# Kernel tuning notes

Measured on AMD Instinct MI355X. Metric: run time of the kernel, lower is better.

## Reference

```python
import jax, jax.numpy as jnp
import numpy as np

B, Nq, C, H = 1, 300, 256, 8
h, w = 32, 32
HW = h * w
HID = 512  # rpe_hidden_dim
HD = C // H


def setup_inputs() -> dict:
    key = jax.random.key(0)
    ks = jax.random.split(key, 16)
    s = 0.02
    inp = {
        "raw_query": jax.random.normal(ks[0], (B, Nq, C), jnp.float32),
        "query_pos": jax.random.normal(ks[1], (B, Nq, C), jnp.float32),
        "reference_points": jax.random.uniform(ks[2], (B, Nq, 2), jnp.float32),
        "raw_src": jax.random.normal(ks[3], (B, HW, C), jnp.float32),
        "src_pos_embed": jax.random.normal(ks[4], (B, HW, C), jnp.float32),
        "Wq": jax.random.normal(ks[5], (C, C), jnp.float32) * s,
        "bq": jnp.zeros((C,), jnp.float32),
        "Wk": jax.random.normal(ks[6], (C, C), jnp.float32) * s,
        "bk": jnp.zeros((C,), jnp.float32),
        "Wv": jax.random.normal(ks[7], (C, C), jnp.float32) * s,
        "bv": jnp.zeros((C,), jnp.float32),
        "Wo": jax.random.normal(ks[8], (C, C), jnp.float32) * s,
        "bo": jnp.zeros((C,), jnp.float32),
        "W1": jax.random.normal(ks[9], (HID, 2), jnp.float32),   # cpb MLP layer 1
        "b1": jnp.zeros((HID,), jnp.float32),
        "W2": jax.random.normal(ks[10], (H, HID), jnp.float32) * s,  # cpb MLP layer 2 (no bias)
        "input_spatial_shapes": np.array([[h, w]], dtype=np.int64),
    }
    return inp


def _key_positions(hh, ww):
    ys = (jnp.arange(hh, dtype=jnp.float32) + 0.5) / hh
    xs = (jnp.arange(ww, dtype=jnp.float32) + 0.5) / ww
    yy, xx = jnp.meshgrid(ys, xs, indexing="ij")  # row-major: idx = y*w + x
    return jnp.stack([xx.ravel(), yy.ravel()], axis=-1)  # [HW, 2] (x, y)


def reference(raw_query, query_pos, reference_points, raw_src, src_pos_embed,
              Wq, bq, Wk, bk, Wv, bv, Wo, bo, W1, b1, W2, input_spatial_shapes):
    hh, ww = int(input_spatial_shapes[0, 0]), int(input_spatial_shapes[0, 1])
    scale = HD ** (-0.5)
    queries = raw_query + query_pos                      # [B,Nq,C]
    memory = raw_src + src_pos_embed                     # [B,HW,C]

    q = (queries @ Wq.T + bq).reshape(B, Nq, H, HD)
    k = (memory @ Wk.T + bk).reshape(B, hh * ww, H, HD)
    v = (memory @ Wv.T + bv).reshape(B, hh * ww, H, HD)

    logits = jnp.einsum("bqhd,bkhd->bhqk", q, k) * scale  # [B,H,Nq,HW]

    key_pos = _key_positions(hh, ww)                      # [HW,2]
    delta = reference_points[:, :, None, :] - key_pos[None, None]  # [B,Nq,HW,2]
    hid = jax.nn.relu(jnp.einsum("bqkc,hc->bqkh", delta, W1) + b1)  # [B,Nq,HW,HID]
    bias = jnp.einsum("bqkf,hf->bhqk", hid, W2)           # [B,H,Nq,HW]

    attn = jax.nn.softmax(logits + bias, axis=-1)
    out = jnp.einsum("bhqk,bkhd->bqhd", attn, v).reshape(B, Nq, C)
    return out @ Wo.T + bo
```

## Files before the change

kernel.cpp:

```cpp
#include <hip/hip_runtime.h>
#include <hip/hip_fp16.h>
#include <stdint.h>

#define NQ   300
#define CDIM 256
#define NH   8
#define HD   32
#define HWK  1024
#define HIDD 512

typedef __attribute__((ext_vector_type(8))) _Float16 f16x8;
typedef __attribute__((ext_vector_type(2))) _Float16 h2v;
typedef __attribute__((ext_vector_type(4))) float f32x4;

#define QB_OFF   0
#define KB_OFF   153600
#define VT_OFF   677888
#define PO_OFF   1202176
#define PL_OFF   3659776
#define A16_OFF  3736576
#define NX_OFF   4043776
#define NY_OFF   4044800
#define W2_OFF   4045824

__device__ __forceinline__ short f16b(float x){
  _Float16 h = (_Float16)x;
  return __builtin_bit_cast(short, h);
}

__device__ __forceinline__ uint32_t pk_f16(float a, float b){
  auto r = __builtin_amdgcn_cvt_pkrtz(a, b);
  return __builtin_bit_cast(uint32_t, r);
}

__global__ __launch_bounds__(256) void proj_kernel(
    const float* __restrict__ rq, const float* __restrict__ qp,
    const float* __restrict__ rs, const float* __restrict__ spe,
    const float* __restrict__ Wq, const float* __restrict__ bq,
    const float* __restrict__ Wk, const float* __restrict__ bk,
    const float* __restrict__ Wv, const float* __restrict__ bv,
    const float* __restrict__ refp, const float* __restrict__ W1,
    const float* __restrict__ b1, const float* __restrict__ W2,
    char* __restrict__ ws)
{
  int bxid = blockIdx.x;
  __shared__ __align__(16) float At[32][20];
  __shared__ float Wl[32][129];

  if (bxid >= 294){
    int idx = (bxid - 294) * 256 + threadIdx.x;
    short* a16  = (short*)(ws + A16_OFF);
    short* nx16 = (short*)(ws + NX_OFF);
    short* ny16 = (short*)(ws + NY_OFF);
    short* w216 = (short*)(ws + W2_OFF);
    if (idx < NQ*HIDD){
      int q = idx >> 9, f = idx & 511;
      float2 w = ((const float2*)W1)[f];
      float a = fmaf(w.x, refp[2*q], fmaf(w.y, refp[2*q+1], b1[f]));
      a16[idx] = f16b(a);
    } else {
      int j = idx - NQ*HIDD;
      if (j < HIDD){
        float2 w = ((const float2*)W1)[j];
        nx16[j] = f16b(-w.x);
        ny16[j] = f16b(-w.y);
      } else if (j < HIDD + NH*HIDD){
        int e = j - HIDD;
        w216[e] = f16b(W2[e]);
      }
    }
    return;
  }

  int tile = bxid >> 1, half = bxid & 1;
  const float *in1, *in2, *W, *bias;
  int r0, M, mode;
  if (tile < 19){
    in1 = rq; in2 = qp; W = Wq; bias = bq; r0 = tile*16; M = NQ; mode = 0;
  } else if (tile < 83){
    in1 = rs; in2 = spe; W = Wk; bias = bk; r0 = (tile-19)*16; M = HWK; mode = 1;
  } else {
    in1 = rs; in2 = spe; W = Wv; bias = bv; r0 = (tile-83)*16; M = HWK; mode = 2;
  }
  int tid = threadIdx.x;
  int n_loc = tid & 127;
  int rg = tid >> 7;
  int n = half*128 + n_loc;
  float acc[8];
  float bv_ = bias[n];
  #pragma unroll
  for (int i=0;i<8;i++) acc[i] = bv_;

  for (int c0 = 0; c0 < CDIM; c0 += 32){
    __syncthreads();
    for (int e = tid; e < 512; e += 256){
      int r = e >> 5, c = e & 31;
      int gr = r0 + r; if (gr >= M) gr = M - 1;
      At[c][r] = in1[gr*CDIM + c0 + c] + in2[gr*CDIM + c0 + c];
    }
    for (int e = tid; e < 4096; e += 256){
      int c = e & 31, nn = e >> 5;
      Wl[c][nn] = W[(half*128 + nn)*CDIM + c0 + c];
    }
    __syncthreads();
    #pragma unroll
    for (int c = 0; c < 32; c++){
      float w = Wl[c][n_loc];
      const float4* ap = (const float4*)&At[c][rg*8];
      float4 a0 = ap[0], a1 = ap[1];
      acc[0] = fmaf(a0.x, w, acc[0]);
      acc[1] = fmaf(a0.y, w, acc[1]);
      acc[2] = fmaf(a0.z, w, acc[2]);
      acc[3] = fmaf(a0.w, w, acc[3]);
      acc[4] = fmaf(a1.x, w, acc[4]);
      acc[5] = fmaf(a1.y, w, acc[5]);
      acc[6] = fmaf(a1.z, w, acc[6]);
      acc[7] = fmaf(a1.w, w, acc[7]);
    }
  }

  if (mode == 0){
    short* qb = (short*)(ws + QB_OFF);
    const float s = 0.17677669529663687f;
    #pragma unroll
    for (int i=0;i<8;i++){
      int gr = r0 + rg*8 + i;
      if (gr < M) qb[gr*CDIM + n] = f16b(acc[i]*s);
    }
  } else if (mode == 1){
    short* kb = (short*)(ws + KB_OFF);
    int h = n >> 5, d = n & 31;
    #pragma unroll
    for (int i=0;i<8;i++){
      int gr = r0 + rg*8 + i;
      if (gr < M) kb[((size_t)h*HWK + gr)*HD + d] = f16b(acc[i]);
    }
  } else {
    short* vt = (short*)(ws + VT_OFF);
    uint32_t p[4];
    #pragma unroll
    for (int i=0;i<4;i++) p[i] = pk_f16(acc[2*i], acc[2*i+1]);
    *(uint4*)(vt + n*HWK + r0 + rg*8) = make_uint4(p[0], p[1], p[2], p[3]);
  }
}

__global__ __launch_bounds__(256, 4) void fused_kernel(
    const short* __restrict__ a16, const short* __restrict__ nx16,
    const short* __restrict__ ny16, const short* __restrict__ w216,
    const short* __restrict__ qb, const short* __restrict__ kb,
    const short* __restrict__ vt, float* __restrict__ po,
    float* __restrict__ pl)
{
  int bid = blockIdx.x;
  int q0 = (bid >> 3) * 2, kr = bid & 7;
  int tid = threadIdx.x, wave = tid >> 6, lane = tid & 63;
  int n = lane & 15, qd = lane >> 4;

  __shared__ __align__(16) _Float16 nwx[HIDD];
  __shared__ __align__(16) char pool[8192];
  __shared__ __align__(16) _Float16 w2l[NH][520];
  __shared__ __align__(16) _Float16 pb[2][NH][136];
  __shared__ float lsum[4][16];
  _Float16 (*c1s)[4][HIDD] = (_Float16 (*)[4][HIDD])pool;
  float (*part)[4][NH][32] = (float (*)[4][NH][32])pool;

  {
    int f0 = tid * 2;
    h2v ny2 = *(const h2v*)(ny16 + f0);
    h2v nx2 = *(const h2v*)(nx16 + f0);
    *(h2v*)&nwx[f0] = nx2;
    #pragma unroll
    for (int qq = 0; qq < 2; qq++){
      h2v a2 = *(const h2v*)(a16 + (q0+qq)*HIDD + f0);
      #pragma unroll
      for (int r = 0; r < 4; r++){
        _Float16 kyh = (_Float16)(((float)(kr*4 + r) + 0.5f) * (1.0f/32.0f));
        h2v ky2 = {kyh, kyh};
        *(h2v*)&c1s[qq][r][f0] = ny2 * ky2 + a2;
      }
    }
  }
  for (int e = tid; e < 512; e += 256){
    int r = e >> 6, c = e & 63;
    *(f16x8*)&w2l[r][c*8] = *(const f16x8*)(w216 + r*HIDD + c*8);
  }
  f16x8 qfrag = *(const f16x8*)(qb + (q0 + (n >> 3))*CDIM + (n & 7)*HD + qd*8);
  f16x8 qm[NH];
  #pragma unroll
  for (int h = 0; h < NH; h++){
    f16x8 z = {0,0,0,0,0,0,0,0};
    qm[h] = ((n & 7) == h) ? qfrag : z;
  }
  __syncthreads();

  const int kyrow = kr*4 + wave;
  const int kbase = kyrow * 32;

  f32x4 acc1[2] = {{0.f,0.f,0.f,0.f},{0.f,0.f,0.f,0.f}};
  #pragma unroll
  for (int t = 0; t < 2; t++){
    int k0 = kbase + t*16;
    #pragma unroll
    for (int h = 0; h < NH; h++){
      f16x8 af = *(const f16x8*)(kb + ((size_t)h*HWK + k0 + n)*HD + qd*8);
      acc1[t] = __builtin_amdgcn_mfma_f32_16x16x32_f16(af, qm[h], acc1[t], 0, 0, 0);
    }
  }

  _Float16 kxAh = (_Float16)(((float)n + 0.5f) * (1.0f/32.0f));
  _Float16 kxBh = (_Float16)(((float)n + 16.5f) * (1.0f/32.0f));
  f16x8 kxA8, kxB8, z8;
  #pragma unroll
  for (int j = 0; j < 8; j++){ kxA8[j] = kxAh; kxB8[j] = kxBh; z8[j] = (_Float16)0.f; }
  f32x4 accb[2][2];
  accb[0][0] = acc1[0]; accb[0][1] = acc1[1];
  accb[1][0] = acc1[0]; accb[1][1] = acc1[1];
  const _Float16* c1r0 = &c1s[0][wave][0];
  const _Float16* c1r1 = &c1s[1][wave][0];
  #pragma unroll 4
  for (int kc = 0; kc < 16; kc++){
    int f0 = kc*32 + qd*8;
    f16x8 c10 = *(const f16x8*)(c1r0 + f0);
    f16x8 c11 = *(const f16x8*)(c1r1 + f0);
    f16x8 wxv = *(const f16x8*)(&nwx[f0]);
    f16x8 bfr = *(const f16x8*)(&w2l[n & 7][f0]);
    #pragma unroll
    for (int t = 0; t < 2; t++){
      f16x8 kx8 = t ? kxB8 : kxA8;
      f16x8 e0 = __builtin_elementwise_max(wxv * kx8 + c10, z8);
      accb[0][t] = __builtin_amdgcn_mfma_f32_16x16x32_f16(e0, bfr, accb[0][t], 0, 0, 0);
      f16x8 e1 = __builtin_elementwise_max(wxv * kx8 + c11, z8);
      accb[1][t] = __builtin_amdgcn_mfma_f32_16x16x32_f16(e1, bfr, accb[1][t], 0, 0, 0);
    }
  }

  int qsel = n >> 3, hsel = n & 7;
  float lacc = 0.f;
  #pragma unroll
  for (int t = 0; t < 2; t++){
    f32x4 a = qsel ? accb[1][t] : accb[0][t];
    float e0 = __expf(a[0]);
    float e1 = __expf(a[1]);
    float e2 = __expf(a[2]);
    float e3 = __expf(a[3]);
    uint2 p2;
    p2.x = pk_f16(e0, e1);
    p2.y = pk_f16(e2, e3);
    *(uint2*)&pb[qsel][hsel][wave*32 + t*16 + qd*4] = p2;
    float s = e0 + e1 + e2 + e3;
    s += __shfl_xor(s, 16);
    s += __shfl_xor(s, 32);
    lacc += s;
  }
  if (lane < 16) lsum[wave][lane] = lacc;

  #pragma unroll
  for (int h = 0; h < NH; h++){
    int kl = wave*32 + qd*8;
    f16x8 pa = *(const f16x8*)&pb[n & 1][h][kl];
    f16x8 v0 = *(const f16x8*)(vt + ((size_t)(h*HD +      n))*HWK + kr*128 + kl);
    f16x8 v1 = *(const f16x8*)(vt + ((size_t)(h*HD + 16 + n))*HWK + kr*128 + kl);
    f32x4 o0 = {0.f,0.f,0.f,0.f}, o1 = {0.f,0.f,0.f,0.f};
    o0 = __builtin_amdgcn_mfma_f32_16x16x32_f16(pa, v0, o0, 0, 0, 0);
    o1 = __builtin_amdgcn_mfma_f32_16x16x32_f16(pa, v1, o1, 0, 0, 0);
    if (qd == 0){
      part[0][wave][h][n]      = o0[0];
      part[1][wave][h][n]      = o0[1];
      part[0][wave][h][16 + n] = o1[0];
      part[1][wave][h][16 + n] = o1[1];
    }
  }
  __syncthreads();

  {
    int h = tid >> 5, d = tid & 31;
    #pragma unroll
    for (int qq = 0; qq < 2; qq++){
      float s = part[qq][0][h][d] + part[qq][1][h][d]
              + part[qq][2][h][d] + part[qq][3][h][d];
      po[((size_t)kr*NQ + q0 + qq)*CDIM + tid] = s;
    }
    if (tid < 16){
      float s = lsum[0][tid] + lsum[1][tid] + lsum[2][tid] + lsum[3][tid];
      pl[((size_t)kr*NQ + q0 + (tid >> 3))*NH + (tid & 7)] = s;
    }
  }
}

__global__ __launch_bounds__(256) void outproj_kernel(
    const float* __restrict__ po, const float* __restrict__ pl,
    const float* __restrict__ Wo, const float* __restrict__ bo,
    float* __restrict__ dout)
{
  int q = blockIdx.x;
  int tid = threadIdx.x;
  __shared__ __align__(16) float a_lds[CDIM];
  __shared__ float linv[NH];

  float s = 0.f;
  #pragma unroll
  for (int p = 0; p < 8; p++) s += po[((size_t)p*NQ + q)*CDIM + tid];

  if (tid < 64){
    int p = tid >> 3, h = tid & 7;
    float l = pl[((size_t)p*NQ + q)*NH + h];
    l += __shfl_xor(l, 8);
    l += __shfl_xor(l, 16);
    l += __shfl_xor(l, 32);
    if (p == 0) linv[h] = 1.0f / l;
  }
  __syncthreads();
  a_lds[tid] = s * linv[tid >> 5];
  __syncthreads();

  const float4* wrow = (const float4*)(Wo + (size_t)tid*CDIM);
  const float4* av = (const float4*)a_lds;
  float acc0 = bo[tid], acc1 = 0.f, acc2 = 0.f, acc3 = 0.f;
  #pragma unroll 4
  for (int c = 0; c < 64; c += 4){
    float4 w0 = wrow[c+0], a0 = av[c+0];
    float4 w1 = wrow[c+1], a1 = av[c+1];
    float4 w2 = wrow[c+2], a2 = av[c+2];
    float4 w3 = wrow[c+3], a3 = av[c+3];
    acc0 = fmaf(w0.x,a0.x,fmaf(w0.y,a0.y,fmaf(w0.z,a0.z,fmaf(w0.w,a0.w,acc0))));
    acc1 = fmaf(w1.x,a1.x,fmaf(w1.y,a1.y,fmaf(w1.z,a1.z,fmaf(w1.w,a1.w,acc1))));
    acc2 = fmaf(w2.x,a2.x,fmaf(w2.y,a2.y,fmaf(w2.z,a2.z,fmaf(w2.w,a2.w,acc2))));
    acc3 = fmaf(w3.x,a3.x,fmaf(w3.y,a3.y,fmaf(w3.z,a3.z,fmaf(w3.w,a3.w,acc3))));
  }
  dout[(size_t)q*CDIM + tid] = acc0 + acc1 + acc2 + acc3;
}

extern "C" void kernel_launch(void* const* d_in, const int* in_sizes, int n_in,
                              void* d_out, int out_size, void* d_ws, size_t ws_size,
                              hipStream_t stream)
{
  const float* rq  = (const float*)d_in[0];
  const float* qp  = (const float*)d_in[1];
  const float* rp  = (const float*)d_in[2];
  const float* rs  = (const float*)d_in[3];
  const float* spe = (const float*)d_in[4];
  const float* Wq  = (const float*)d_in[5];
  const float* bq  = (const float*)d_in[6];
  const float* Wk  = (const float*)d_in[7];
  const float* bk  = (const float*)d_in[8];
  const float* Wv  = (const float*)d_in[9];
  const float* bv  = (const float*)d_in[10];
  const float* Wo  = (const float*)d_in[11];
  const float* bo  = (const float*)d_in[12];
  const float* W1  = (const float*)d_in[13];
  const float* b1  = (const float*)d_in[14];
  const float* W2  = (const float*)d_in[15];
  char* ws = (char*)d_ws;
  float* dout = (float*)d_out;

  proj_kernel<<<912, 256, 0, stream>>>(rq, qp, rs, spe, Wq, bq, Wk, bk,
      Wv, bv, rp, W1, b1, W2, ws);
  fused_kernel<<<1200, 256, 0, stream>>>((const short*)(ws + A16_OFF),
      (const short*)(ws + NX_OFF), (const short*)(ws + NY_OFF),
      (const short*)(ws + W2_OFF), (const short*)(ws + QB_OFF),
      (const short*)(ws + KB_OFF), (const short*)(ws + VT_OFF),
      (float*)(ws + PO_OFF), (float*)(ws + PL_OFF));
  outproj_kernel<<<300, 256, 0, stream>>>((const float*)(ws + PO_OFF),
      (const float*)(ws + PL_OFF), Wo, bo, dout);
}
```

Measured before the change: 144.3 us.

## Fuse output projection into attention kernel via last-block atomic counter

Removes the separate outproj kernel launch. Each query-pair group keeps an atomic counter, and the last of its 8 key-range blocks to finish reduces the partial outputs and applies the Wo projection in place. This saves a kernel launch and the tail gap between kernels, but adds a memset launch, threadfences, atomics, and extra serial work in the last block of each group.

```diff
diff --git a/kernel.cpp b/kernel.cpp
--- a/kernel.cpp
+++ b/kernel.cpp
@@ -22,6 +22,7 @@
 #define NX_OFF   4043776
 #define NY_OFF   4044800
 #define W2_OFF   4045824
+#define QC_OFF   4056064
 
 __device__ __forceinline__ short f16b(float x){
   _Float16 h = (_Float16)x;
@@ -144,12 +145,56 @@
   }
 }
 
+__device__ __forceinline__ void dev_outproj(int q,
+    const float* __restrict__ po, const float* __restrict__ pl,
+    const float* __restrict__ Wo, const float* __restrict__ bo,
+    float* __restrict__ dout, char* __restrict__ smem)
+{
+  int tid = threadIdx.x;
+  float* a_lds = (float*)smem;
+  float* linv  = (float*)(smem + 1024);
+
+  float s = 0.f;
+  #pragma unroll
+  for (int p = 0; p < 8; p++) s += po[((size_t)p*NQ + q)*CDIM + tid];
+
+  if (tid < 64){
+    int p = tid >> 3, h = tid & 7;
+    float l = pl[((size_t)p*NQ + q)*NH + h];
+    l += __shfl_xor(l, 8);
+    l += __shfl_xor(l, 16);
+    l += __shfl_xor(l, 32);
+    if (p == 0) linv[h] = 1.0f / l;
+  }
+  __syncthreads();
+  a_lds[tid] = s * linv[tid >> 5];
+  __syncthreads();
+
+  const float4* wrow = (const float4*)(Wo + (size_t)tid*CDIM);
+  const float4* av = (const float4*)a_lds;
+  float acc0 = bo[tid], acc1 = 0.f, acc2 = 0.f, acc3 = 0.f;
+  #pragma unroll 4
+  for (int c = 0; c < 64; c += 4){
+    float4 w0 = wrow[c+0], a0 = av[c+0];
+    float4 w1 = wrow[c+1], a1 = av[c+1];
+    float4 w2 = wrow[c+2], a2 = av[c+2];
+    float4 w3 = wrow[c+3], a3 = av[c+3];
+    acc0 = fmaf(w0.x,a0.x,fmaf(w0.y,a0.y,fmaf(w0.z,a0.z,fmaf(w0.w,a0.w,acc0))));
+    acc1 = fmaf(w1.x,a1.x,fmaf(w1.y,a1.y,fmaf(w1.z,a1.z,fmaf(w1.w,a1.w,acc1))));
+    acc2 = fmaf(w2.x,a2.x,fmaf(w2.y,a2.y,fmaf(w2.z,a2.z,fmaf(w2.w,a2.w,acc2))));
+    acc3 = fmaf(w3.x,a3.x,fmaf(w3.y,a3.y,fmaf(w3.z,a3.z,fmaf(w3.w,a3.w,acc3))));
+  }
+  dout[(size_t)q*CDIM + tid] = acc0 + acc1 + acc2 + acc3;
+}
+
 __global__ __launch_bounds__(256, 4) void fused_kernel(
     const short* __restrict__ a16, const short* __restrict__ nx16,
     const short* __restrict__ ny16, const short* __restrict__ w216,
     const short* __restrict__ qb, const short* __restrict__ kb,
     const short* __restrict__ vt, float* __restrict__ po,
-    float* __restrict__ pl)
+    float* __restrict__ pl,
+    const float* __restrict__ Wo, const float* __restrict__ bo,
+    float* __restrict__ dout, unsigned* __restrict__ qcnt)
 {
   int bid = blockIdx.x;
   int q0 = (bid >> 3) * 2, kr = bid & 7;
@@ -161,6 +206,7 @@
   __shared__ __align__(16) _Float16 w2l[NH][520];
   __shared__ __align__(16) _Float16 pb[2][NH][136];
   __shared__ float lsum[4][16];
+  __shared__ unsigned last_flag;
   _Float16 (*c1s)[4][HIDD] = (_Float16 (*)[4][HIDD])pool;
   float (*part)[4][NH][32] = (float (*)[4][NH][32])pool;
 
@@ -285,49 +331,21 @@
       pl[((size_t)kr*NQ + q0 + (tid >> 3))*NH + (tid & 7)] = s;
     }
   }
-}
-
-__global__ __launch_bounds__(256) void outproj_kernel(
-    const float* __restrict__ po, const float* __restrict__ pl,
-    const float* __restrict__ Wo, const float* __restrict__ bo,
-    float* __restrict__ dout)
-{
-  int q = blockIdx.x;
-  int tid = threadIdx.x;
-  __shared__ __align__(16) float a_lds[CDIM];
-  __shared__ float linv[NH];
-
-  float s = 0.f;
-  #pragma unroll
-  for (int p = 0; p < 8; p++) s += po[((size_t)p*NQ + q)*CDIM + tid];
-
-  if (tid < 64){
-    int p = tid >> 3, h = tid & 7;
-    float l = pl[((size_t)p*NQ + q)*NH + h];
-    l += __shfl_xor(l, 8);
-    l += __shfl_xor(l, 16);
-    l += __shfl_xor(l, 32);
-    if (p == 0) linv[h] = 1.0f / l;
-  }
-  __syncthreads();
-  a_lds[tid] = s * linv[tid >> 5];
-  __syncthreads();
-
-  const float4* wrow = (const float4*)(Wo + (size_t)tid*CDIM);
-  const float4* av = (const float4*)a_lds;
-  float acc0 = bo[tid], acc1 = 0.f, acc2 = 0.f, acc3 = 0.f;
-  #pragma unroll 4
-  for (int c = 0; c < 64; c += 4){
-    float4 w0 = wrow[c+0], a0 = av[c+0];
-    float4 w1 = wrow[c+1], a1 = av[c+1];
-    float4 w2 = wrow[c+2], a2 = av[c+2];
-    float4 w3 = wrow[c+3], a3 = av[c+3];
-    acc0 = fmaf(w0.x,a0.x,fmaf(w0.y,a0.y,fmaf(w0.z,a0.z,fmaf(w0.w,a0.w,acc0))));
-    acc1 = fmaf(w1.x,a1.x,fmaf(w1.y,a1.y,fmaf(w1.z,a1.z,fmaf(w1.w,a1.w,acc1))));
-    acc2 = fmaf(w2.x,a2.x,fmaf(w2.y,a2.y,fmaf(w2.z,a2.z,fmaf(w2.w,a2.w,acc2))));
-    acc3 = fmaf(w3.x,a3.x,fmaf(w3.y,a3.y,fmaf(w3.z,a3.z,fmaf(w3.w,a3.w,acc3))));
-  }
-  dout[(size_t)q*CDIM + tid] = acc0 + acc1 + acc2 + acc3;
+
+  __threadfence();
+  __syncthreads();
+  if (tid == 0){
+    unsigned prev = __hip_atomic_fetch_add(&qcnt[bid >> 3], 1u,
+        __ATOMIC_ACQ_REL, __HIP_MEMORY_SCOPE_AGENT);
+    last_flag = (prev == 7u) ? 1u : 0u;
+  }
+  __syncthreads();
+  if (last_flag){
+    __threadfence();
+    dev_outproj(q0,     po, pl, Wo, bo, dout, pool);
+    __syncthreads();
+    dev_outproj(q0 + 1, po, pl, Wo, bo, dout, pool);
+  }
 }
 
 extern "C" void kernel_launch(void* const* d_in, const int* in_sizes, int n_in,
@@ -353,13 +371,14 @@
   char* ws = (char*)d_ws;
   float* dout = (float*)d_out;
 
+  hipMemsetAsync(ws + QC_OFF, 0, 1024, stream);
+
   proj_kernel<<<912, 256, 0, stream>>>(rq, qp, rs, spe, Wq, bq, Wk, bk,
       Wv, bv, rp, W1, b1, W2, ws);
   fused_kernel<<<1200, 256, 0, stream>>>((const short*)(ws + A16_OFF),
       (const short*)(ws + NX_OFF), (const short*)(ws + NY_OFF),
       (const short*)(ws + W2_OFF), (const short*)(ws + QB_OFF),
       (const short*)(ws + KB_OFF), (const short*)(ws + VT_OFF),
-      (float*)(ws + PO_OFF), (float*)(ws + PL_OFF));
-  outproj_kernel<<<300, 256, 0, stream>>>((const float*)(ws + PO_OFF),
-      (const float*)(ws + PL_OFF), Wo, bo, dout);
-}
+      (float*)(ws + PO_OFF), (float*)(ws + PL_OFF),
+      Wo, bo, dout, (unsigned*)(ws + QC_OFF));
+}
```

Measured after the change: 319.2 us. +121.1%, slower.

## Fuse output projection into attention kernel, looping over key splits per block

Applied to the files above, without the earlier changes.

Each block now processes one query pair across all eight key-row chunks in a loop, accumulating outputs and softmax sums in shared memory. It then applies the normalization and the Wo projection directly, removing the separate outproj kernel and the partial-sum workspace round trip. This trades away grid parallelism (150 blocks instead of 1200) and adds per-iteration barriers. That risks leaving much of the GPU idle.

```diff
diff --git a/kernel.cpp b/kernel.cpp
--- a/kernel.cpp
+++ b/kernel.cpp
@@ -16,8 +16,6 @@
 #define QB_OFF   0
 #define KB_OFF   153600
 #define VT_OFF   677888
-#define PO_OFF   1202176
-#define PL_OFF   3659776
 #define A16_OFF  3736576
 #define NX_OFF   4043776
 #define NY_OFF   4044800
@@ -144,15 +142,16 @@
   }
 }
 
-__global__ __launch_bounds__(256, 4) void fused_kernel(
+__global__ __launch_bounds__(256) void fused_kernel(
     const short* __restrict__ a16, const short* __restrict__ nx16,
     const short* __restrict__ ny16, const short* __restrict__ w216,
     const short* __restrict__ qb, const short* __restrict__ kb,
-    const short* __restrict__ vt, float* __restrict__ po,
-    float* __restrict__ pl)
+    const short* __restrict__ vt,
+    const float* __restrict__ Wo, const float* __restrict__ bo,
+    float* __restrict__ dout)
 {
   int bid = blockIdx.x;
-  int q0 = (bid >> 3) * 2, kr = bid & 7;
+  int q0 = bid * 2;
   int tid = threadIdx.x, wave = tid >> 6, lane = tid & 63;
   int n = lane & 15, qd = lane >> 4;
 
@@ -161,25 +160,18 @@
   __shared__ __align__(16) _Float16 w2l[NH][520];
   __shared__ __align__(16) _Float16 pb[2][NH][136];
   __shared__ float lsum[4][16];
+  __shared__ __align__(16) float o_acc[2][CDIM];
+  __shared__ float linv_s[16];
   _Float16 (*c1s)[4][HIDD] = (_Float16 (*)[4][HIDD])pool;
   float (*part)[4][NH][32] = (float (*)[4][NH][32])pool;
 
-  {
-    int f0 = tid * 2;
-    h2v ny2 = *(const h2v*)(ny16 + f0);
-    h2v nx2 = *(const h2v*)(nx16 + f0);
-    *(h2v*)&nwx[f0] = nx2;
-    #pragma unroll
-    for (int qq = 0; qq < 2; qq++){
-      h2v a2 = *(const h2v*)(a16 + (q0+qq)*HIDD + f0);
-      #pragma unroll
-      for (int r = 0; r < 4; r++){
-        _Float16 kyh = (_Float16)(((float)(kr*4 + r) + 0.5f) * (1.0f/32.0f));
-        h2v ky2 = {kyh, kyh};
-        *(h2v*)&c1s[qq][r][f0] = ny2 * ky2 + a2;
-      }
-    }
-  }
+  int f0 = tid * 2;
+  h2v ny2 = *(const h2v*)(ny16 + f0);
+  h2v nx2 = *(const h2v*)(nx16 + f0);
+  *(h2v*)&nwx[f0] = nx2;
+  h2v a2q[2];
+  a2q[0] = *(const h2v*)(a16 + q0*HIDD + f0);
+  a2q[1] = *(const h2v*)(a16 + (q0+1)*HIDD + f0);
   for (int e = tid; e < 512; e += 256){
     int r = e >> 6, c = e & 63;
     *(f16x8*)&w2l[r][c*8] = *(const f16x8*)(w216 + r*HIDD + c*8);
@@ -191,143 +183,135 @@
     f16x8 z = {0,0,0,0,0,0,0,0};
     qm[h] = ((n & 7) == h) ? qfrag : z;
   }
-  __syncthreads();
-
-  const int kyrow = kr*4 + wave;
-  const int kbase = kyrow * 32;
-
-  f32x4 acc1[2] = {{0.f,0.f,0.f,0.f},{0.f,0.f,0.f,0.f}};
-  #pragma unroll
-  for (int t = 0; t < 2; t++){
-    int k0 = kbase + t*16;
-    #pragma unroll
-    for (int h = 0; h < NH; h++){
-      f16x8 af = *(const f16x8*)(kb + ((size_t)h*HWK + k0 + n)*HD + qd*8);
-      acc1[t] = __builtin_amdgcn_mfma_f32_16x16x32_f16(af, qm[h], acc1[t], 0, 0, 0);
-    }
-  }
-
   _Float16 kxAh = (_Float16)(((float)n + 0.5f) * (1.0f/32.0f));
   _Float16 kxBh = (_Float16)(((float)n + 16.5f) * (1.0f/32.0f));
   f16x8 kxA8, kxB8, z8;
   #pragma unroll
   for (int j = 0; j < 8; j++){ kxA8[j] = kxAh; kxB8[j] = kxBh; z8[j] = (_Float16)0.f; }
-  f32x4 accb[2][2];
-  accb[0][0] = acc1[0]; accb[0][1] = acc1[1];
-  accb[1][0] = acc1[0]; accb[1][1] = acc1[1];
-  const _Float16* c1r0 = &c1s[0][wave][0];
-  const _Float16* c1r1 = &c1s[1][wave][0];
-  #pragma unroll 4
-  for (int kc = 0; kc < 16; kc++){
-    int f0 = kc*32 + qd*8;
-    f16x8 c10 = *(const f16x8*)(c1r0 + f0);
-    f16x8 c11 = *(const f16x8*)(c1r1 + f0);
-    f16x8 wxv = *(const f16x8*)(&nwx[f0]);
-    f16x8 bfr = *(const f16x8*)(&w2l[n & 7][f0]);
+
+  o_acc[0][tid] = 0.f;
+  o_acc[1][tid] = 0.f;
+
+  float lacc = 0.f;
+
+  for (int kr = 0; kr < 8; kr++){
+    #pragma unroll
+    for (int r = 0; r < 4; r++){
+      _Float16 kyh = (_Float16)(((float)(kr*4 + r) + 0.5f) * (1.0f/32.0f));
+      h2v ky2 = {kyh, kyh};
+      *(h2v*)&c1s[0][r][f0] = ny2 * ky2 + a2q[0];
+      *(h2v*)&c1s[1][r][f0] = ny2 * ky2 + a2q[1];
+    }
+    __syncthreads();
+
+    const int kyrow = kr*4 + wave;
+    const int kbase = kyrow * 32;
+
+    f32x4 acc1[2] = {{0.f,0.f,0.f,0.f},{0.f,0.f,0.f,0.f}};
     #pragma unroll
     for (int t = 0; t < 2; t++){
-      f16x8 kx8 = t ? kxB8 : kxA8;
-      f16x8 e0 = __builtin_elementwise_max(wxv * kx8 + c10, z8);
-      accb[0][t] = __builtin_amdgcn_mfma_f32_16x16x32_f16(e0, bfr, accb[0][t], 0, 0, 0);
-      f16x8 e1 = __builtin_elementwise_max(wxv * kx8 + c11, z8);
-      accb[1][t] = __builtin_amdgcn_mfma_f32_16x16x32_f16(e1, bfr, accb[1][t], 0, 0, 0);
-    }
-  }
-
-  int qsel = n >> 3, hsel = n & 7;
-  float lacc = 0.f;
-  #pragma unroll
-  for (int t = 0; t < 2; t++){
-    f32x4 a = qsel ? accb[1][t] : accb[0][t];
-    float e0 = __expf(a[0]);
-    float e1 = __expf(a[1]);
-    float e2 = __expf(a[2]);
-    float e3 = __expf(a[3]);
-    uint2 p2;
-    p2.x = pk_f16(e0, e1);
-    p2.y = pk_f16(e2, e3);
-    *(uint2*)&pb[qsel][hsel][wave*32 + t*16 + qd*4] = p2;
-    float s = e0 + e1 + e2 + e3;
-    s += __shfl_xor(s, 16);
-    s += __shfl_xor(s, 32);
-    lacc += s;
-  }
+      int k0 = kbase + t*16;
+      #pragma unroll
+      for (int h = 0; h < NH; h++){
+        f16x8 af = *(const f16x8*)(kb + ((size_t)h*HWK + k0 + n)*HD + qd*8);
+        acc1[t] = __builtin_amdgcn_mfma_f32_16x16x32_f16(af, qm[h], acc1[t], 0, 0, 0);
+      }
+    }
+
+    f32x4 accb[2][2];
+    accb[0][0] = acc1[0]; accb[0][1] = acc1[1];
+    accb[1][0] = acc1[0]; accb[1][1] = acc1[1];
+    const _Float16* c1r0 = &c1s[0][wave][0];
+    const _Float16* c1r1 = &c1s[1][wave][0];
+    #pragma unroll 4
+    for (int kc = 0; kc < 16; kc++){
+      int ff = kc*32 + qd*8;
+      f16x8 c10 = *(const f16x8*)(c1r0 + ff);
+      f16x8 c11 = *(const f16x8*)(c1r1 + ff);
+      f16x8 wxv = *(const f16x8*)(&nwx[ff]);
+      f16x8 bfr = *(const f16x8*)(&w2l[n & 7][ff]);
+      #pragma unroll
+      for (int t = 0; t < 2; t++){
+        f16x8 kx8 = t ? kxB8 : kxA8;
+        f16x8 e0 = __builtin_elementwise_max(wxv * kx8 + c10, z8);
+        accb[0][t] = __builtin_amdgcn_mfma_f32_16x16x32_f16(e0, bfr, accb[0][t], 0, 0, 0);
+        f16x8 e1 = __builtin_elementwise_max(wxv * kx8 + c11, z8);
+        accb[1][t] = __builtin_amdgcn_mfma_f32_16x16x32_f16(e1, bfr, accb[1][t], 0, 0, 0);
+      }
+    }
+
+    int qsel = n >> 3, hsel = n & 7;
+    #pragma unroll
+    for (int t = 0; t < 2; t++){
+      f32x4 a = qsel ? accb[1][t] : accb[0][t];
+      float e0 = __expf(a[0]);
+      float e1 = __expf(a[1]);
+      float e2 = __expf(a[2]);
+      float e3 = __expf(a[3]);
+      uint2 p2;
+      p2.x = pk_f16(e0, e1);
+      p2.y = pk_f16(e2, e3);
+      *(uint2*)&pb[qsel][hsel][wave*32 + t*16 + qd*4] = p2;
+      float s = e0 + e1 + e2 + e3;
+      s += __shfl_xor(s, 16);
+      s += __shfl_xor(s, 32);
+      lacc += s;
+    }
+
+    #pragma unroll
+    for (int h = 0; h < NH; h++){
+      int kl = wave*32 + qd*8;
+      f16x8 pa = *(const f16x8*)&pb[n & 1][h][kl];
+      f16x8 v0 = *(const f16x8*)(vt + ((size_t)(h*HD +      n))*HWK + kr*128 + kl);
+      f16x8 v1 = *(const f16x8*)(vt + ((size_t)(h*HD + 16 + n))*HWK + kr*128 + kl);
+      f32x4 o0 = {0.f,0.f,0.f,0.f}, o1 = {0.f,0.f,0.f,0.f};
+      o0 = __builtin_amdgcn_mfma_f32_16x16x32_f16(pa, v0, o0, 0, 0, 0);
+      o1 = __builtin_amdgcn_mfma_f32_16x16x32_f16(pa, v1, o1, 0, 0, 0);
+      if (qd == 0){
+        part[0][wave][h][n]      = o0[0];
+        part[1][wave][h][n]      = o0[1];
+        part[0][wave][h][16 + n] = o1[0];
+        part[1][wave][h][16 + n] = o1[1];
+      }
+    }
+    __syncthreads();
+
+    {
+      int h = tid >> 5, d = tid & 31;
+      #pragma unroll
+      for (int qq = 0; qq < 2; qq++){
+        o_acc[qq][tid] += part[qq][0][h][d] + part[qq][1][h][d]
+                        + part[qq][2][h][d] + part[qq][3][h][d];
+      }
+    }
+    __syncthreads();
+  }
+
   if (lane < 16) lsum[wave][lane] = lacc;
-
-  #pragma unroll
-  for (int h = 0; h < NH; h++){
-    int kl = wave*32 + qd*8;
-    f16x8 pa = *(const f16x8*)&pb[n & 1][h][kl];
-    f16x8 v0 = *(const f16x8*)(vt + ((size_t)(h*HD +      n))*HWK + kr*128 + kl);
-    f16x8 v1 = *(const f16x8*)(vt + ((size_t)(h*HD + 16 + n))*HWK + kr*128 + kl);
-    f32x4 o0 = {0.f,0.f,0.f,0.f}, o1 = {0.f,0.f,0.f,0.f};
-    o0 = __builtin_amdgcn_mfma_f32_16x16x32_f16(pa, v0, o0, 0, 0, 0);
-    o1 = __builtin_amdgcn_mfma_f32_16x16x32_f16(pa, v1, o1, 0, 0, 0);
-    if (qd == 0){
-      part[0][wave][h][n]      = o0[0];
-      part[1][wave][h][n]      = o0[1];
-      part[0][wave][h][16 + n] = o1[0];
-      part[1][wave][h][16 + n] = o1[1];
-    }
-  }
   __syncthreads();
-
-  {
-    int h = tid >> 5, d = tid & 31;
-    #pragma unroll
-    for (int qq = 0; qq < 2; qq++){
-      float s = part[qq][0][h][d] + part[qq][1][h][d]
-              + part[qq][2][h][d] + part[qq][3][h][d];
-      po[((size_t)kr*NQ + q0 + qq)*CDIM + tid] = s;
-    }
-    if (tid < 16){
-      float s = lsum[0][tid] + lsum[1][tid] + lsum[2][tid] + lsum[3][tid];
-      pl[((size_t)kr*NQ + q0 + (tid >> 3))*NH + (tid & 7)] = s;
-    }
-  }
-}
-
-__global__ __launch_bounds__(256) void outproj_kernel(
-    const float* __restrict__ po, const float* __restrict__ pl,
-    const float* __restrict__ Wo, const float* __restrict__ bo,
-    float* __restrict__ dout)
-{
-  int q = blockIdx.x;
-  int tid = threadIdx.x;
-  __shared__ __align__(16) float a_lds[CDIM];
-  __shared__ float linv[NH];
-
-  float s = 0.f;
-  #pragma unroll
-  for (int p = 0; p < 8; p++) s += po[((size_t)p*NQ + q)*CDIM + tid];
-
-  if (tid < 64){
-    int p = tid >> 3, h = tid & 7;
-    float l = pl[((size_t)p*NQ + q)*NH + h];
-    l += __shfl_xor(l, 8);
-    l += __shfl_xor(l, 16);
-    l += __shfl_xor(l, 32);
-    if (p == 0) linv[h] = 1.0f / l;
+  if (tid < 16){
+    float l = lsum[0][tid] + lsum[1][tid] + lsum[2][tid] + lsum[3][tid];
+    linv_s[tid] = 1.0f / l;
   }
   __syncthreads();
-  a_lds[tid] = s * linv[tid >> 5];
+  o_acc[0][tid] *= linv_s[tid >> 5];
+  o_acc[1][tid] *= linv_s[8 + (tid >> 5)];
   __syncthreads();
 
   const float4* wrow = (const float4*)(Wo + (size_t)tid*CDIM);
-  const float4* av = (const float4*)a_lds;
-  float acc0 = bo[tid], acc1 = 0.f, acc2 = 0.f, acc3 = 0.f;
-  #pragma unroll 4
-  for (int c = 0; c < 64; c += 4){
-    float4 w0 = wrow[c+0], a0 = av[c+0];
-    float4 w1 = wrow[c+1], a1 = av[c+1];
-    float4 w2 = wrow[c+2], a2 = av[c+2];
-    float4 w3 = wrow[c+3], a3 = av[c+3];
-    acc0 = fmaf(w0.x,a0.x,fmaf(w0.y,a0.y,fmaf(w0.z,a0.z,fmaf(w0.w,a0.w,acc0))));
-    acc1 = fmaf(w1.x,a1.x,fmaf(w1.y,a1.y,fmaf(w1.z,a1.z,fmaf(w1.w,a1.w,acc1))));
-    acc2 = fmaf(w2.x,a2.x,fmaf(w2.y,a2.y,fmaf(w2.z,a2.z,fmaf(w2.w,a2.w,acc2))));
-    acc3 = fmaf(w3.x,a3.x,fmaf(w3.y,a3.y,fmaf(w3.z,a3.z,fmaf(w3.w,a3.w,acc3))));
-  }
-  dout[(size_t)q*CDIM + tid] = acc0 + acc1 + acc2 + acc3;
+  const float4* av0 = (const float4*)&o_acc[0][0];
+  const float4* av1 = (const float4*)&o_acc[1][0];
+  float s0 = bo[tid], s1 = s0;
+  #pragma unroll 8
+  for (int c = 0; c < 64; c++){
+    float4 w = wrow[c];
+    float4 a0 = av0[c];
+    float4 a1 = av1[c];
+    s0 = fmaf(w.x,a0.x,fmaf(w.y,a0.y,fmaf(w.z,a0.z,fmaf(w.w,a0.w,s0))));
+    s1 = fmaf(w.x,a1.x,fmaf(w.y,a1.y,fmaf(w.z,a1.z,fmaf(w.w,a1.w,s1))));
+  }
+  dout[(size_t)q0*CDIM + tid]       = s0;
+  dout[(size_t)(q0+1)*CDIM + tid]   = s1;
 }
 
 extern "C" void kernel_launch(void* const* d_in, const int* in_sizes, int n_in,
@@ -355,11 +339,9 @@
 
   proj_kernel<<<912, 256, 0, stream>>>(rq, qp, rs, spe, Wq, bq, Wk, bk,
       Wv, bv, rp, W1, b1, W2, ws);
-  fused_kernel<<<1200, 256, 0, stream>>>((const short*)(ws + A16_OFF),
+  fused_kernel<<<150, 256, 0, stream>>>((const short*)(ws + A16_OFF),
       (const short*)(ws + NX_OFF), (const short*)(ws + NY_OFF),
       (const short*)(ws + W2_OFF), (const short*)(ws + QB_OFF),
       (const short*)(ws + KB_OFF), (const short*)(ws + VT_OFF),
-      (float*)(ws + PO_OFF), (float*)(ws + PL_OFF));
-  outproj_kernel<<<300, 256, 0, stream>>>((const float*)(ws + PO_OFF),
-      (const float*)(ws + PL_OFF), Wo, bo, dout);
-}
+      Wo, bo, dout);
+}
```

After: 196.2 us. +36.0%, slower.

## Process one query per block instead of two, doubling grid and occupancy

Applied to the files above, without the earlier changes.

The fused attention kernel now handles a single query per block, so the launch grows from 1200 to 2400 blocks and launch bounds ask for 8 blocks per CU. Shared memory and per-thread accumulators are halved, and the bias MLP inner loop issues half the MFMAs per block. The intent is more parallelism and occupancy to hide latency. In exchange, half the MFMA rows carry no useful query, and each block repeats the K/V loads and per-block setup twice as often.

```diff
diff --git a/kernel.cpp b/kernel.cpp
--- a/kernel.cpp
+++ b/kernel.cpp
@@ -144,7 +144,7 @@
   }
 }
 
-__global__ __launch_bounds__(256, 4) void fused_kernel(
+__global__ __launch_bounds__(256, 8) void fused_kernel(
     const short* __restrict__ a16, const short* __restrict__ nx16,
     const short* __restrict__ ny16, const short* __restrict__ w216,
     const short* __restrict__ qb, const short* __restrict__ kb,
@@ -152,45 +152,39 @@
     float* __restrict__ pl)
 {
   int bid = blockIdx.x;
-  int q0 = (bid >> 3) * 2, kr = bid & 7;
+  int q = bid >> 3, kr = bid & 7;
   int tid = threadIdx.x, wave = tid >> 6, lane = tid & 63;
   int n = lane & 15, qd = lane >> 4;
 
   __shared__ __align__(16) _Float16 nwx[HIDD];
-  __shared__ __align__(16) char pool[8192];
+  __shared__ __align__(16) char pool[4096];
   __shared__ __align__(16) _Float16 w2l[NH][520];
-  __shared__ __align__(16) _Float16 pb[2][NH][136];
+  __shared__ __align__(16) _Float16 pb[NH][136];
   __shared__ float lsum[4][16];
-  _Float16 (*c1s)[4][HIDD] = (_Float16 (*)[4][HIDD])pool;
-  float (*part)[4][NH][32] = (float (*)[4][NH][32])pool;
+  _Float16 (*c1s)[HIDD] = (_Float16 (*)[HIDD])pool;
+  float (*part)[NH][32] = (float (*)[NH][32])pool;
 
   {
     int f0 = tid * 2;
     h2v ny2 = *(const h2v*)(ny16 + f0);
     h2v nx2 = *(const h2v*)(nx16 + f0);
     *(h2v*)&nwx[f0] = nx2;
-    #pragma unroll
-    for (int qq = 0; qq < 2; qq++){
-      h2v a2 = *(const h2v*)(a16 + (q0+qq)*HIDD + f0);
-      #pragma unroll
-      for (int r = 0; r < 4; r++){
-        _Float16 kyh = (_Float16)(((float)(kr*4 + r) + 0.5f) * (1.0f/32.0f));
-        h2v ky2 = {kyh, kyh};
-        *(h2v*)&c1s[qq][r][f0] = ny2 * ky2 + a2;
-      }
+    h2v a2 = *(const h2v*)(a16 + q*HIDD + f0);
+    #pragma unroll
+    for (int r = 0; r < 4; r++){
+      _Float16 kyh = (_Float16)(((float)(kr*4 + r) + 0.5f) * (1.0f/32.0f));
+      h2v ky2 = {kyh, kyh};
+      *(h2v*)&c1s[r][f0] = ny2 * ky2 + a2;
     }
   }
   for (int e = tid; e < 512; e += 256){
     int r = e >> 6, c = e & 63;
     *(f16x8*)&w2l[r][c*8] = *(const f16x8*)(w216 + r*HIDD + c*8);
   }
-  f16x8 qfrag = *(const f16x8*)(qb + (q0 + (n >> 3))*CDIM + (n & 7)*HD + qd*8);
-  f16x8 qm[NH];
-  #pragma unroll
-  for (int h = 0; h < NH; h++){
-    f16x8 z = {0,0,0,0,0,0,0,0};
-    qm[h] = ((n & 7) == h) ? qfrag : z;
-  }
+  f16x8 qfrag = *(const f16x8*)(qb + q*CDIM + (n & 7)*HD + qd*8);
+  f16x8 z8f;
+  #pragma unroll
+  for (int j = 0; j < 8; j++) z8f[j] = (_Float16)0.f;
   __syncthreads();
 
   const int kyrow = kr*4 + wave;
@@ -198,47 +192,42 @@
 
   f32x4 acc1[2] = {{0.f,0.f,0.f,0.f},{0.f,0.f,0.f,0.f}};
   #pragma unroll
-  for (int t = 0; t < 2; t++){
-    int k0 = kbase + t*16;
-    #pragma unroll
-    for (int h = 0; h < NH; h++){
+  for (int h = 0; h < NH; h++){
+    f16x8 bq8 = ((n & 7) == h && n < 8) ? qfrag : z8f;
+    #pragma unroll
+    for (int t = 0; t < 2; t++){
+      int k0 = kbase + t*16;
       f16x8 af = *(const f16x8*)(kb + ((size_t)h*HWK + k0 + n)*HD + qd*8);
-      acc1[t] = __builtin_amdgcn_mfma_f32_16x16x32_f16(af, qm[h], acc1[t], 0, 0, 0);
+      acc1[t] = __builtin_amdgcn_mfma_f32_16x16x32_f16(af, bq8, acc1[t], 0, 0, 0);
     }
   }
 
   _Float16 kxAh = (_Float16)(((float)n + 0.5f) * (1.0f/32.0f));
   _Float16 kxBh = (_Float16)(((float)n + 16.5f) * (1.0f/32.0f));
-  f16x8 kxA8, kxB8, z8;
-  #pragma unroll
-  for (int j = 0; j < 8; j++){ kxA8[j] = kxAh; kxB8[j] = kxBh; z8[j] = (_Float16)0.f; }
-  f32x4 accb[2][2];
-  accb[0][0] = acc1[0]; accb[0][1] = acc1[1];
-  accb[1][0] = acc1[0]; accb[1][1] = acc1[1];
-  const _Float16* c1r0 = &c1s[0][wave][0];
-  const _Float16* c1r1 = &c1s[1][wave][0];
+  f16x8 kxA8, kxB8;
+  #pragma unroll
+  for (int j = 0; j < 8; j++){ kxA8[j] = kxAh; kxB8[j] = kxBh; }
+  f32x4 accb[2];
+  accb[0] = acc1[0]; accb[1] = acc1[1];
+  const _Float16* c1r = &c1s[wave][0];
   #pragma unroll 4
   for (int kc = 0; kc < 16; kc++){
-    int f0 = kc*32 + qd*8;
-    f16x8 c10 = *(const f16x8*)(c1r0 + f0);
-    f16x8 c11 = *(const f16x8*)(c1r1 + f0);
-    f16x8 wxv = *(const f16x8*)(&nwx[f0]);
-    f16x8 bfr = *(const f16x8*)(&w2l[n & 7][f0]);
+    int ff = kc*32 + qd*8;
+    f16x8 c10 = *(const f16x8*)(c1r + ff);
+    f16x8 wxv = *(const f16x8*)(&nwx[ff]);
+    f16x8 bfr = *(const f16x8*)(&w2l[n & 7][ff]);
     #pragma unroll
     for (int t = 0; t < 2; t++){
       f16x8 kx8 = t ? kxB8 : kxA8;
-      f16x8 e0 = __builtin_elementwise_max(wxv * kx8 + c10, z8);
-      accb[0][t] = __builtin_amdgcn_mfma_f32_16x16x32_f16(e0, bfr, accb[0][t], 0, 0, 0);
-      f16x8 e1 = __builtin_elementwise_max(wxv * kx8 + c11, z8);
-      accb[1][t] = __builtin_amdgcn_mfma_f32_16x16x32_f16(e1, bfr, accb[1][t], 0, 0, 0);
-    }
-  }
-
-  int qsel = n >> 3, hsel = n & 7;
+      f16x8 e0 = __builtin_elementwise_max(wxv * kx8 + c10, z8f);
+      accb[t] = __builtin_amdgcn_mfma_f32_16x16x32_f16(e0, bfr, accb[t], 0, 0, 0);
+    }
+  }
+
   float lacc = 0.f;
   #pragma unroll
   for (int t = 0; t < 2; t++){
-    f32x4 a = qsel ? accb[1][t] : accb[0][t];
+    f32x4 a = accb[t];
     float e0 = __expf(a[0]);
     float e1 = __expf(a[1]);
     float e2 = __expf(a[2]);
@@ -246,43 +235,39 @@
     uint2 p2;
     p2.x = pk_f16(e0, e1);
     p2.y = pk_f16(e2, e3);
-    *(uint2*)&pb[qsel][hsel][wave*32 + t*16 + qd*4] = p2;
     float s = e0 + e1 + e2 + e3;
     s += __shfl_xor(s, 16);
     s += __shfl_xor(s, 32);
-    lacc += s;
-  }
-  if (lane < 16) lsum[wave][lane] = lacc;
+    if (n < 8){
+      *(uint2*)&pb[n][wave*32 + t*16 + qd*4] = p2;
+      lacc += s;
+    }
+  }
+  if (lane < 8) lsum[wave][lane] = lacc;
 
   #pragma unroll
   for (int h = 0; h < NH; h++){
     int kl = wave*32 + qd*8;
-    f16x8 pa = *(const f16x8*)&pb[n & 1][h][kl];
+    f16x8 pa = *(const f16x8*)&pb[h][kl];
     f16x8 v0 = *(const f16x8*)(vt + ((size_t)(h*HD +      n))*HWK + kr*128 + kl);
     f16x8 v1 = *(const f16x8*)(vt + ((size_t)(h*HD + 16 + n))*HWK + kr*128 + kl);
     f32x4 o0 = {0.f,0.f,0.f,0.f}, o1 = {0.f,0.f,0.f,0.f};
     o0 = __builtin_amdgcn_mfma_f32_16x16x32_f16(pa, v0, o0, 0, 0, 0);
     o1 = __builtin_amdgcn_mfma_f32_16x16x32_f16(pa, v1, o1, 0, 0, 0);
     if (qd == 0){
-      part[0][wave][h][n]      = o0[0];
-      part[1][wave][h][n]      = o0[1];
-      part[0][wave][h][16 + n] = o1[0];
-      part[1][wave][h][16 + n] = o1[1];
+      part[wave][h][n]      = o0[0];
+      part[wave][h][16 + n] = o1[0];
     }
   }
   __syncthreads();
 
   {
     int h = tid >> 5, d = tid & 31;
-    #pragma unroll
-    for (int qq = 0; qq < 2; qq++){
-      float s = part[qq][0][h][d] + part[qq][1][h][d]
-              + part[qq][2][h][d] + part[qq][3][h][d];
-      po[((size_t)kr*NQ + q0 + qq)*CDIM + tid] = s;
-    }
-    if (tid < 16){
-      float s = lsum[0][tid] + lsum[1][tid] + lsum[2][tid] + lsum[3][tid];
-      pl[((size_t)kr*NQ + q0 + (tid >> 3))*NH + (tid & 7)] = s;
+    float s = part[0][h][d] + part[1][h][d] + part[2][h][d] + part[3][h][d];
+    po[((size_t)kr*NQ + q)*CDIM + tid] = s;
+    if (tid < 8){
+      float l = lsum[0][tid] + lsum[1][tid] + lsum[2][tid] + lsum[3][tid];
+      pl[((size_t)kr*NQ + q)*NH + tid] = l;
     }
   }
 }
@@ -355,7 +340,7 @@
 
   proj_kernel<<<912, 256, 0, stream>>>(rq, qp, rs, spe, Wq, bq, Wk, bk,
       Wv, bv, rp, W1, b1, W2, ws);
-  fused_kernel<<<1200, 256, 0, stream>>>((const short*)(ws + A16_OFF),
+  fused_kernel<<<2400, 256, 0, stream>>>((const short*)(ws + A16_OFF),
       (const short*)(ws + NX_OFF), (const short*)(ws + NY_OFF),
       (const short*)(ws + W2_OFF), (const short*)(ws + QB_OFF),
       (const short*)(ws + KB_OFF), (const short*)(ws + VT_OFF),
```

Result: slower. 159.2 us (+10.3%).
